# Kernel tuning notes

Hardware: AMD Instinct MI355X
Metric: run time of the kernel (lower is better)

Reference implementation:

```python
import jax, jax.numpy as jnp
import numpy as np

BS, H, S, DK = 4, 16, 1024, 64
NEG = -1e9  # finite large-negative for additive causal mask


def setup_inputs() -> dict:
    key = jax.random.key(0)
    kq, kk, kv, kp, kl = jax.random.split(key, 5)
    q = jax.random.normal(kq, (BS, H, S, DK), dtype=jnp.float32)
    k = jax.random.normal(kk, (BS, H, DK, S), dtype=jnp.float32)  # K pre-transposed per docstring
    v = jax.random.normal(kv, (BS, H, S, DK), dtype=jnp.float32)
    prev = jax.random.normal(kp, (BS, H, S, S), dtype=jnp.float32) * 0.1  # residual attention bias
    # additive causal mask (float branch of attn_mask handling)
    causal = jnp.triu(jnp.ones((S, S), dtype=bool), k=1)
    attn_mask = jnp.where(causal, jnp.float32(NEG), jnp.float32(0.0))
    # padding mask: each batch row pads a random trailing suffix
    lengths = jax.random.randint(kl, (BS,), S // 2, S + 1)
    key_padding_mask = jnp.arange(S)[None, :] >= lengths[:, None]  # True = padded
    return {"q": q, "k": k, "v": v, "prev": prev,
            "attn_mask": attn_mask, "key_padding_mask": key_padding_mask}


def reference(q, k, v, prev, attn_mask, key_padding_mask):
    d_k = q.shape[-1]
    # scores: [bs, h, q_len, seq_len]; k is already [bs, h, d_k, seq_len]
    scores = jnp.einsum('bhqd,bhds->bhqs', q, k) / jnp.sqrt(jnp.float32(d_k))
    scores = scores + prev                      # residual attention bias
    scores = scores + attn_mask                 # float additive attn_mask branch
    # key_padding_mask: [bs, seq_len] -> [bs, 1, 1, seq_len], True -> -inf
    scores = jnp.where(key_padding_mask[:, None, None, :], -jnp.inf, scores)
    attn = jax.nn.softmax(scores, axis=-1)      # [bs, h, q_len, seq_len]
    context = jnp.einsum('bhqs,bhsd->bhqd', attn, v)
    return context, attn
```

## Files before the change

kernel.cpp:

```cpp
#include <hip/hip_runtime.h>

typedef _Float16 f16;
typedef f16 f16x8 __attribute__((ext_vector_type(8)));
typedef f16 f16x4 __attribute__((ext_vector_type(4)));
typedef float f32x4 __attribute__((ext_vector_type(4)));

#define BSZ 4
#define NH 16
#define SEQ 1024
#define DKD 64
#define QB 16
#define LOG2E 1.44269504088896340736f

#define KP_ELEMS ((size_t)BSZ * NH * SEQ * DKD)
#define WS_LEN_OFF  (2 * KP_ELEMS * sizeof(f16))

__global__ __launch_bounds__(256, 4)
void prepack_kernel(const float* __restrict__ kg,
                    const float* __restrict__ vg,
                    const int*   __restrict__ kpm,
                    f16* __restrict__ wsf,
                    int* __restrict__ lenw)
{
    __shared__ float lds[64][65];
    __shared__ int smode, slen[BSZ];
    const int tid  = threadIdx.x;
    const int st   = blockIdx.x;
    const int bh   = blockIdx.y;
    const int task = blockIdx.z;

    if (task == 0) {
        const float* src = kg + (size_t)bh * SEQ * DKD + (size_t)st * 64;
        f16* dst = wsf + (size_t)bh * SEQ * DKD + (size_t)st * 64 * 64;
        const int rr = tid >> 2, cb = (tid & 3) * 16;
        #pragma unroll
        for (int i = 0; i < 4; ++i) {
            f32x4 x = *(const f32x4*)(src + (size_t)rr * SEQ + cb + i * 4);
            lds[rr][cb + i * 4 + 0] = x[0];
            lds[rr][cb + i * 4 + 1] = x[1];
            lds[rr][cb + i * 4 + 2] = x[2];
            lds[rr][cb + i * 4 + 3] = x[3];
        }
        __syncthreads();
        const int c = tid >> 2, rb = (tid & 3) * 16;
        f16 tmp[16];
        #pragma unroll
        for (int i = 0; i < 16; ++i) tmp[i] = (f16)lds[rb + i][c];
        *(f16x8*)(dst + (size_t)c * 64 + rb)     = *(f16x8*)&tmp[0];
        *(f16x8*)(dst + (size_t)c * 64 + rb + 8) = *(f16x8*)&tmp[8];
    } else {
        const float* src = vg + (size_t)bh * SEQ * DKD + (size_t)st * 64 * 64;
        f16* dst = wsf + KP_ELEMS + (size_t)bh * SEQ * DKD;
        const int rr = tid >> 2, cb = (tid & 3) * 16;
        #pragma unroll
        for (int i = 0; i < 4; ++i) {
            f32x4 x = *(const f32x4*)(src + (size_t)rr * 64 + cb + i * 4);
            lds[rr][cb + i * 4 + 0] = x[0];
            lds[rr][cb + i * 4 + 1] = x[1];
            lds[rr][cb + i * 4 + 2] = x[2];
            lds[rr][cb + i * 4 + 3] = x[3];
        }
        __syncthreads();
        const int dv = tid & 63, sq0 = tid >> 6;
        #pragma unroll
        for (int i = 0; i < 4; ++i) {
            const int sq = sq0 + 4 * i;
            f16x4 v;
            #pragma unroll
            for (int j = 0; j < 4; ++j) v[j] = (f16)lds[sq * 4 + j][dv];
            *(f16x4*)(dst + ((size_t)(st * 16 + sq) * 256 + dv * 4)) = v;
        }
    }

    if (st == 0 && bh == 0 && task == 0) {
        if (tid < BSZ) slen[tid] = SEQ;
        if (tid == BSZ) smode = 0;
        __syncthreads();
        {
            const unsigned int* w32 = (const unsigned int*)kpm;
            int bad = 0;
            #pragma unroll
            for (int j = 0; j < 4; ++j) {
                unsigned int w = w32[tid * 4 + j];
                if (w != 0u && w != 1u && w != 0x3F800000u) bad = 1;
            }
            if (bad) atomicOr(&smode, 1);
        }
        __syncthreads();
        for (int b = 0; b < BSZ; ++b) {
            int m0 = SEQ;
            if (smode == 0) {
                const unsigned int* w32 = (const unsigned int*)kpm + b * SEQ;
                #pragma unroll
                for (int j = 0; j < 4; ++j) {
                    int i = tid * 4 + j;
                    if (w32[i] != 0u && i < m0) m0 = i;
                }
            } else {
                const unsigned char* u8 = (const unsigned char*)kpm + b * SEQ;
                #pragma unroll
                for (int j = 0; j < 4; ++j) {
                    int i = tid * 4 + j;
                    if (u8[i] != 0 && i < m0) m0 = i;
                }
            }
            if (m0 < SEQ) atomicMin(&slen[b], m0);
        }
        __syncthreads();
        if (tid < BSZ) lenw[tid] = slen[tid];
    }
}

__global__ __launch_bounds__(256, 4)
void sdpa_mono_kernel(const float* __restrict__ qg,
                      const float* __restrict__ pg,
                      const f16*  __restrict__ wsf,
                      const int*  __restrict__ lenw,
                      float* __restrict__ out_ctx,
                      float* __restrict__ out_attn)
{
    __shared__ __align__(16) f16 Elds[QB * SEQ];
    __shared__ float redp[QB * 65];
    __shared__ float rs_part[4][QB];
#define REDP(row, dv) redp[(row) * 65 + (dv)]

    const int tid  = threadIdx.x;
    const int wave = tid >> 6;
    const int lane = tid & 63;
    const int lo   = lane & 15;
    const int hi   = lane >> 4;

    const int bid  = blockIdx.x;
    const int nid  = (bid & 7) * 512 + (bid >> 3);
    const int bh   = nid >> 6;
    const int qblk = 63 - (nid & 63);
    const int b    = bh >> 4;
    const int q0   = qblk * QB;

    const int len  = lenw[b];
    const int smax = min(q0 + QB, len);
    const int nT   = (smax + 63) >> 6;

    const size_t qkvbase = (size_t)bh * SEQ * DKD;
    const f16* kpp = wsf + qkvbase;
    const f16* vpk = wsf + KP_ELEMS + qkvbase + (wave * 4 + hi) * 256 + lo * 4;
    const float* pp = pg + (size_t)bh * SEQ * SEQ + (size_t)(q0 + lo) * SEQ + wave * 16 + hi * 4;
    const int qrow = q0 + lo;

    f16x8 qb0, qb1;
    {
        const float* src = qg + qkvbase + (size_t)qrow * DKD + hi * 8;
        #pragma unroll
        for (int j = 0; j < 8; ++j) qb0[j] = (f16)(src[j] * 0.125f);
        #pragma unroll
        for (int j = 0; j < 8; ++j) qb1[j] = (f16)(src[32 + j] * 0.125f);
    }

    f32x4 accP[4] = {{0.f,0.f,0.f,0.f},{0.f,0.f,0.f,0.f},{0.f,0.f,0.f,0.f},{0.f,0.f,0.f,0.f}};
    float rsl = 0.f;

    f32x4 bP[16];
    f16x8 bK0[2], bK1[2];
    f16x4 bV[2][4];

#define LOADKV(SL, T) do {                                                      \
    const int c0_ = (T) * 64 + wave * 16;                                       \
    bK0[SL] = *(const f16x8*)(kpp + (size_t)(c0_ + lo) * DKD + hi * 8);         \
    bK1[SL] = *(const f16x8*)(kpp + (size_t)(c0_ + lo) * DKD + 32 + hi * 8);    \
    bV[SL][0] = *(const f16x4*)(vpk + (T) * 4096);                              \
    bV[SL][1] = *(const f16x4*)(vpk + (T) * 4096 + 64);                         \
    bV[SL][2] = *(const f16x4*)(vpk + (T) * 4096 + 128);                        \
    bV[SL][3] = *(const f16x4*)(vpk + (T) * 4096 + 192);                        \
} while (0)

    LOADKV(0, 0);
    if (1 < nT) LOADKV(1, 1);
    #pragma unroll
    for (int i = 0; i < 16; ++i)
        if (i < nT) bP[i] = __builtin_nontemporal_load((const f32x4*)(pp + i * 64));

    #pragma unroll
    for (int t = 0; t < 16; ++t) {
        if (t < nT) {
            const f32x4 pv = bP[t];
            f32x4 accS = {0.f, 0.f, 0.f, 0.f};
            accS = __builtin_amdgcn_mfma_f32_16x16x32_f16(bK0[t & 1], qb0, accS, 0, 0, 0);
            accS = __builtin_amdgcn_mfma_f32_16x16x32_f16(bK1[t & 1], qb1, accS, 0, 0, 0);
            const int c0_ = t * 64 + wave * 16;
            f16x4 ev;
            #pragma unroll
            for (int r = 0; r < 4; ++r) {
                const int scol = c0_ + hi * 4 + r;
                const float sc = accS[r] + pv[r];
                float e = (scol <= qrow && scol < len) ? exp2f(sc * LOG2E) : 0.f;
                rsl += e;
                ev[r] = (f16)e;
            }
            *(f16x4*)&Elds[lo * SEQ + ((c0_ + hi * 4) ^ ((lo & 7) << 3))] = ev;
            accP[0] = __builtin_amdgcn_mfma_f32_16x16x16f16(ev, bV[t & 1][0], accP[0], 0, 0, 0);
            accP[1] = __builtin_amdgcn_mfma_f32_16x16x16f16(ev, bV[t & 1][1], accP[1], 0, 0, 0);
            accP[2] = __builtin_amdgcn_mfma_f32_16x16x16f16(ev, bV[t & 1][2], accP[2], 0, 0, 0);
            accP[3] = __builtin_amdgcn_mfma_f32_16x16x16f16(ev, bV[t & 1][3], accP[3], 0, 0, 0);
            if (t + 2 < nT) LOADKV(t & 1, t + 2);
        }
    }
#undef LOADKV

    rsl += __shfl_xor(rsl, 16);
    rsl += __shfl_xor(rsl, 32);
    if (lane < 16) rs_part[wave][lane] = rsl;

    #pragma unroll
    for (int w = 0; w < 4; ++w) {
        __syncthreads();
        if (wave == w) {
            #pragma unroll
            for (int dvb = 0; dvb < 4; ++dvb) {
                #pragma unroll
                for (int r = 0; r < 4; ++r) {
                    const int row = hi * 4 + r, dv = dvb * 16 + lo;
                    if (w == 0) REDP(row, dv) = accP[dvb][r];
                    else        REDP(row, dv) += accP[dvb][r];
                }
            }
        }
    }
    __syncthreads();

    float* ctxp = out_ctx + qkvbase + (size_t)q0 * DKD;
    #pragma unroll
    for (int i = 0; i < 4; ++i) {
        const int f = i * 256 + tid;
        const int row = f >> 6, dv = f & 63;
        const float inv = 1.0f / (rs_part[0][row] + rs_part[1][row] + rs_part[2][row] + rs_part[3][row]);
        __builtin_nontemporal_store(REDP(row, dv) * inv, ctxp + f);
    }

    {
        float* ap = out_attn + (size_t)bh * SEQ * SEQ + (size_t)q0 * SEQ;
        const int zlim = nT * 64;
        #pragma unroll
        for (int ro = 0; ro < 4; ++ro) {
            const int row = wave * 4 + ro;
            const float invr = 1.0f / (rs_part[0][row] + rs_part[1][row] + rs_part[2][row] + rs_part[3][row]);
            float* dst = ap + (size_t)row * SEQ;
            #pragma unroll
            for (int it = 0; it < 4; ++it) {
                const int c = it * 256 + lane * 4;
                f32x4 o;
                if (c < zlim) {
                    f16x4 evv = *(const f16x4*)&Elds[row * SEQ + (c ^ ((row & 7) << 3))];
                    o[0] = (float)evv[0] * invr;
                    o[1] = (float)evv[1] * invr;
                    o[2] = (float)evv[2] * invr;
                    o[3] = (float)evv[3] * invr;
                } else {
                    o = (f32x4){0.f, 0.f, 0.f, 0.f};
                }
                __builtin_nontemporal_store(o, (f32x4*)(dst + c));
            }
        }
    }
#undef REDP
}

extern "C" void kernel_launch(void* const* d_in, const int* in_sizes, int n_in,
                              void* d_out, int out_size, void* d_ws, size_t ws_size,
                              hipStream_t stream) {
    const float* q    = (const float*)d_in[0];
    const float* k    = (const float*)d_in[1];
    const float* v    = (const float*)d_in[2];
    const float* prev = (const float*)d_in[3];
    const int*   kpm  = (const int*)d_in[5];

    float* out_ctx  = (float*)d_out;
    float* out_attn = out_ctx + (size_t)BSZ * NH * SEQ * DKD;

    f16* wsf  = (f16*)d_ws;
    int* lenw = (int*)((char*)d_ws + WS_LEN_OFF);

    prepack_kernel<<<dim3(16, 64, 2), 256, 0, stream>>>(k, v, kpm, wsf, lenw);
    sdpa_mono_kernel<<<dim3(64 * 64), 256, 0, stream>>>(q, prev, wsf, lenw, out_ctx, out_attn);
}
```

Before: 158.3 us.

## Halve prev prefetch registers and replace serial wave reduction with fp16 LDS partials

The prefetch of the residual-bias tiles now uses an 8-entry register ring instead of 16, loading the second half of the tiles mid-loop at iteration 4. This frees VGPRs, which may help occupancy. The cross-wave context reduction no longer runs four serialized syncthreads rounds. Waves 1-3 now write fp16 partials to LDS once, and wave 0 sums them with its own accumulators and writes the context. That cuts barriers and LDS traffic, but rounding the partials to fp16 loses precision, and the context store now uses a strided per-lane pattern issued by one wave.

```diff
diff --git a/kernel.cpp b/kernel.cpp
--- a/kernel.cpp
+++ b/kernel.cpp
@@ -120,9 +120,9 @@
                       float* __restrict__ out_attn)
 {
     __shared__ __align__(16) f16 Elds[QB * SEQ];
-    __shared__ float redp[QB * 65];
+    __shared__ f16 redh[3 * QB * 66];
     __shared__ float rs_part[4][QB];
-#define REDP(row, dv) redp[(row) * 65 + (dv)]
+#define REDH(w, row, dv) redh[((w) * QB + (row)) * 66 + (dv)]
 
     const int tid  = threadIdx.x;
     const int wave = tid >> 6;
@@ -159,7 +159,7 @@
     f32x4 accP[4] = {{0.f,0.f,0.f,0.f},{0.f,0.f,0.f,0.f},{0.f,0.f,0.f,0.f},{0.f,0.f,0.f,0.f}};
     float rsl = 0.f;
 
-    f32x4 bP[16];
+    f32x4 bP[8];
     f16x8 bK0[2], bK1[2];
     f16x4 bV[2][4];
 
@@ -176,13 +176,13 @@
     LOADKV(0, 0);
     if (1 < nT) LOADKV(1, 1);
     #pragma unroll
-    for (int i = 0; i < 16; ++i)
+    for (int i = 0; i < 8; ++i)
         if (i < nT) bP[i] = __builtin_nontemporal_load((const f32x4*)(pp + i * 64));
 
     #pragma unroll
     for (int t = 0; t < 16; ++t) {
         if (t < nT) {
-            const f32x4 pv = bP[t];
+            const f32x4 pv = bP[t & 7];
             f32x4 accS = {0.f, 0.f, 0.f, 0.f};
             accS = __builtin_amdgcn_mfma_f32_16x16x32_f16(bK0[t & 1], qb0, accS, 0, 0, 0);
             accS = __builtin_amdgcn_mfma_f32_16x16x32_f16(bK1[t & 1], qb1, accS, 0, 0, 0);
@@ -202,6 +202,11 @@
             accP[2] = __builtin_amdgcn_mfma_f32_16x16x16f16(ev, bV[t & 1][2], accP[2], 0, 0, 0);
             accP[3] = __builtin_amdgcn_mfma_f32_16x16x16f16(ev, bV[t & 1][3], accP[3], 0, 0, 0);
             if (t + 2 < nT) LOADKV(t & 1, t + 2);
+            if (t == 4) {
+                #pragma unroll
+                for (int i = 8; i < 16; ++i)
+                    if (i < nT) bP[i - 8] = __builtin_nontemporal_load((const f32x4*)(pp + i * 64));
+            }
         }
     }
 #undef LOADKV
@@ -210,30 +215,30 @@
     rsl += __shfl_xor(rsl, 32);
     if (lane < 16) rs_part[wave][lane] = rsl;
 
-    #pragma unroll
-    for (int w = 0; w < 4; ++w) {
-        __syncthreads();
-        if (wave == w) {
-            #pragma unroll
-            for (int dvb = 0; dvb < 4; ++dvb) {
-                #pragma unroll
-                for (int r = 0; r < 4; ++r) {
-                    const int row = hi * 4 + r, dv = dvb * 16 + lo;
-                    if (w == 0) REDP(row, dv) = accP[dvb][r];
-                    else        REDP(row, dv) += accP[dvb][r];
-                }
-            }
+    if (wave != 0) {
+        #pragma unroll
+        for (int dvb = 0; dvb < 4; ++dvb) {
+            #pragma unroll
+            for (int r = 0; r < 4; ++r)
+                REDH(wave - 1, hi * 4 + r, dvb * 16 + lo) = (f16)accP[dvb][r];
         }
     }
     __syncthreads();
 
-    float* ctxp = out_ctx + qkvbase + (size_t)q0 * DKD;
-    #pragma unroll
-    for (int i = 0; i < 4; ++i) {
-        const int f = i * 256 + tid;
-        const int row = f >> 6, dv = f & 63;
-        const float inv = 1.0f / (rs_part[0][row] + rs_part[1][row] + rs_part[2][row] + rs_part[3][row]);
-        __builtin_nontemporal_store(REDP(row, dv) * inv, ctxp + f);
+    if (wave == 0) {
+        float* ctxp = out_ctx + qkvbase + (size_t)q0 * DKD;
+        #pragma unroll
+        for (int dvb = 0; dvb < 4; ++dvb) {
+            #pragma unroll
+            for (int r = 0; r < 4; ++r) {
+                const int row = hi * 4 + r, dv = dvb * 16 + lo;
+                const float s = accP[dvb][r] + (float)REDH(0, row, dv)
+                              + (float)REDH(1, row, dv) + (float)REDH(2, row, dv);
+                const float inv = 1.0f / (rs_part[0][row] + rs_part[1][row]
+                                        + rs_part[2][row] + rs_part[3][row]);
+                __builtin_nontemporal_store(s * inv, ctxp + row * DKD + dv);
+            }
+        }
     }
 
     {
@@ -242,7 +247,8 @@
         #pragma unroll
         for (int ro = 0; ro < 4; ++ro) {
             const int row = wave * 4 + ro;
-            const float invr = 1.0f / (rs_part[0][row] + rs_part[1][row] + rs_part[2][row] + rs_part[3][row]);
+            const float invr = 1.0f / (rs_part[0][row] + rs_part[1][row]
+                                     + rs_part[2][row] + rs_part[3][row]);
             float* dst = ap + (size_t)row * SEQ;
             #pragma unroll
             for (int it = 0; it < 4; ++it) {
@@ -261,7 +267,7 @@
             }
         }
     }
-#undef REDP
+#undef REDH
 }
 
 extern "C" void kernel_launch(void* const* d_in, const int* in_sizes, int n_in,
```

Result: faster. 151.1 us (-4.5%).
